# Kernel tuning notes

Measured on AMD Instinct MI355X. Metric: run time of the kernel, lower is better.

The kernel has to match this reference:

```python
import jax, jax.numpy as jnp
import numpy as np

B, L, DM, DH = 8, 2048, 1024, 1024


def setup_inputs() -> dict:
    key = jax.random.key(0)
    ks = jax.random.split(key, 10)
    s_dm = 1.0 / np.sqrt(DM)   # nn.Linear(d_model, *) init bound
    s_dh = 1.0 / np.sqrt(DH)   # nn.Linear(d_hidden, *) init bound
    u = lambda k, shp, s: jax.random.uniform(k, shp, jnp.float32, -s, s)
    return {
        "x": jax.random.normal(ks[0], (B, L, DM), jnp.float32),
        # A scaled by 0.01 so cumprod(exp(delta*A)) stays finite over L=2048
        "A": 0.01 * jax.random.normal(ks[1], (DH,), jnp.float32),
        "Bw": u(ks[2], (DH, DM), s_dm), "Bb": u(ks[3], (DH,), s_dm),
        "Cw": u(ks[4], (DM, DH), s_dh), "Cb": u(ks[5], (DM,), s_dh),
        "Dw": u(ks[6], (DM, DM), s_dm), "Db": u(ks[7], (DM,), s_dm),
        "dw": u(ks[8], (DH, DM), s_dm), "db": u(ks[9], (DH,), s_dm),
    }


def reference(x, A, Bw, Bb, Cw, Cb, Dw, Db, dw, db):
    # x: [B, L, DM]
    delta = jax.nn.softplus(jnp.einsum('bld,hd->blh', x, dw) + db)   # [B,L,DH]
    A_bar = jnp.exp(delta * A)                                        # [B,L,DH]
    B_bar = delta * (jnp.einsum('bld,hd->blh', x, Bw) + Bb)           # [B,L,DH]
    A_cum = jnp.cumprod(A_bar, axis=1)                                # [B,L,DH]
    h = jnp.cumsum(B_bar / A_cum, axis=1) * A_cum                     # [B,L,DH]
    out = jnp.einsum('blh,dh->bld', h, Cw) + Cb \
        + jnp.einsum('bld,ed->ble', x, Dw) + Db                       # [B,L,DM]
    return out
```

## Files before the change

### kernel.cpp

```cpp
#include <hip/hip_runtime.h>
#include <hip/hip_bf16.h>
#include <stdint.h>

#define DMODEL 1024
#define DHID   1024
#define NBATCH 8
#define LSEQ   2048
#define MROWS  (NBATCH * LSEQ)
#define KCAT   2048
#define CH     32
#define NCH    64
#define BH     (NBATCH * DHID)
#define CPT    4

typedef __attribute__((ext_vector_type(8))) short  short8;
typedef __attribute__((ext_vector_type(4))) short  s16x4;
typedef __attribute__((ext_vector_type(8))) __bf16 bf16x8;
typedef __attribute__((ext_vector_type(4))) float  f32x4;

__device__ __forceinline__ unsigned short f2bf(float f) {
  union { float f; unsigned int u; } v; v.f = f;
  unsigned int u = v.u;
  u += 0x7fffu + ((u >> 16) & 1u);
  return (unsigned short)(u >> 16);
}

__device__ __forceinline__ float bf2f(unsigned short s) {
  union { unsigned int u; float f; } v; v.u = ((unsigned int)s) << 16;
  return v.f;
}

__device__ __forceinline__ float softplus_f(float x) {
  return fmaxf(x, 0.f) + log1pf(expf(-fabsf(x)));
}

__device__ __forceinline__ short8 pack8(float4 a, float4 b) {
  short8 o;
  o[0] = (short)f2bf(a.x); o[1] = (short)f2bf(a.y);
  o[2] = (short)f2bf(a.z); o[3] = (short)f2bf(a.w);
  o[4] = (short)f2bf(b.x); o[5] = (short)f2bf(b.y);
  o[6] = (short)f2bf(b.z); o[7] = (short)f2bf(b.w);
  return o;
}

__global__ __launch_bounds__(256)
void cast_all_kernel(const float* __restrict__ x,
                     const float* __restrict__ dw, const float* __restrict__ Bw,
                     const float* __restrict__ Cw, const float* __restrict__ Dw,
                     unsigned short* __restrict__ A2,
                     unsigned short* __restrict__ W1, unsigned short* __restrict__ W2) {
  const size_t MX = (size_t)MROWS * 1024;
  const size_t M1 = (size_t)1024 * 1024;
  size_t i8 = ((size_t)blockIdx.x * 256 + threadIdx.x) * 8;
  if (i8 < MX) {
    size_t row = i8 >> 10; int col = (int)(i8 & 1023);
    const float4* p = (const float4*)(x + i8);
    *(short8*)(A2 + row * (size_t)KCAT + 1024 + col) = pack8(p[0], p[1]);
  } else if (i8 < MX + 2 * M1) {
    size_t k = i8 - MX;
    const float* src = (k < M1) ? (dw + k) : (Bw + k - M1);
    const float4* p = (const float4*)src;
    *(short8*)(W1 + k) = pack8(p[0], p[1]);
  } else {
    size_t k = i8 - MX - 2 * M1;
    size_t d = k >> 11; int c = (int)(k & 2047);
    const float* src = (c < 1024) ? (Cw + d * 1024 + c) : (Dw + d * 1024 + (c - 1024));
    const float4* p = (const float4*)src;
    *(short8*)(W2 + k) = pack8(p[0], p[1]);
  }
}

__device__ __forceinline__ void stage_tile(const unsigned short* g0, int ld,
                                           unsigned short* s0, int t, int lane) {
#pragma unroll
  for (int half = 0; half < 2; ++half) {
    int c = t + half * 256;
    const unsigned short* g = g0 + (size_t)(c >> 2) * ld + (c & 3) * 8;
    unsigned short* s = s0 + ((size_t)(t - lane) + half * 256) * 8;
    __builtin_amdgcn_global_load_lds(
        (const __attribute__((address_space(1))) unsigned int*)g,
        (__attribute__((address_space(3))) unsigned int*)s, 16, 0, 0);
  }
}

__global__ __launch_bounds__(256, 4)
void gemm_bt(const unsigned short* __restrict__ A, int lda,
             const unsigned short* __restrict__ B, int ldb,
             void* __restrict__ Cp, int ldc, int K, int mode,
             const float* __restrict__ bias0, const float* __restrict__ bias1) {
  __shared__ __align__(16) unsigned short As[128 * 32];
  __shared__ __align__(16) unsigned short Bs[128 * 32];
  const int t = threadIdx.x;
  const int lane = t & 63, wave = t >> 6;
  const int quad = lane >> 4, l16 = lane & 15;

  const int Nt = gridDim.x, Mt = gridDim.y;
  int bid = blockIdx.y * Nt + blockIdx.x;
  int xcd = bid & 7;
  int slot = bid >> 3;
  int lm = slot / Nt;
  int ln = slot - lm * Nt;
  const int m0 = (xcd * (Mt >> 3) + lm) * 128;
  const int n0 = ln * 128;

  const int wm = (wave & 1) * 64, wn = (wave >> 1) * 64;

  const unsigned short* Ab = A + (size_t)m0 * lda;
  const unsigned short* Bb = B + (size_t)n0 * ldb;

  f32x4 acc[4][4] = {};

  for (int k0 = 0; k0 < K; k0 += 32) {
    stage_tile(Ab + k0, lda, As, t, lane);
    stage_tile(Bb + k0, ldb, Bs, t, lane);
    __syncthreads();
    short8 af[4], bfr[4];
#pragma unroll
    for (int i = 0; i < 4; ++i)
      af[i] = *(const short8*)(As + ((size_t)(wm + i * 16 + l16)) * 32 + quad * 8);
#pragma unroll
    for (int j = 0; j < 4; ++j)
      bfr[j] = *(const short8*)(Bs + ((size_t)(wn + j * 16 + l16)) * 32 + quad * 8);
#pragma unroll
    for (int i = 0; i < 4; ++i)
#pragma unroll
      for (int j = 0; j < 4; ++j)
        acc[i][j] = __builtin_amdgcn_mfma_f32_16x16x32_bf16(
            __builtin_bit_cast(bf16x8, af[i]),
            __builtin_bit_cast(bf16x8, bfr[j]), acc[i][j], 0, 0, 0);
    __syncthreads();
  }

  if (mode == 0) {
    float* C = (float*)Cp;
#pragma unroll
    for (int i = 0; i < 4; ++i)
#pragma unroll
      for (int j = 0; j < 4; ++j) {
        int n = n0 + wn + j * 16 + l16;
        int mb = m0 + wm + i * 16 + quad * 4;
        float badd = bias0[n] + bias1[n];
#pragma unroll
        for (int r = 0; r < 4; ++r)
          C[(size_t)(mb + r) * ldc + n] = acc[i][j][r] + badd;
      }
  } else {
    unsigned short* C16 = (unsigned short*)Cp;
#pragma unroll
    for (int i = 0; i < 4; ++i)
#pragma unroll
      for (int j = 0; j < 4; ++j) {
        int n = n0 + wn + j * 16 + l16;
        int mb = m0 + wm + i * 16 + quad * 4;
#pragma unroll
        for (int r = 0; r < 4; ++r)
          C16[(size_t)(mb + r) * ldc + n] = f2bf(acc[i][j][r]);
      }
  }
}

__global__ __launch_bounds__(256)
void scan_carry_kernel(unsigned short* __restrict__ G1,
                       const float* __restrict__ Av, const float* __restrict__ Bbv,
                       const float* __restrict__ dbv, float2* __restrict__ carr) {
  int t = blockIdx.x * 256 + threadIdx.x;
  int ho = t & 255, chunk = (t >> 8) & (NCH - 1), b = t >> 14;
  int h0 = ho << 2;
  float4 A0 = *(const float4*)(Av + h0);
  float4 B0 = *(const float4*)(Bbv + h0);
  float4 D0 = *(const float4*)(dbv + h0);
  float Ah[4]  = {A0.x, A0.y, A0.z, A0.w};
  float Bbh[4] = {B0.x, B0.y, B0.z, B0.w};
  float dbh[4] = {D0.x, D0.y, D0.z, D0.w};
  unsigned short* base = G1 + ((size_t)(b * LSEQ + chunk * CH)) * KCAT + h0;
  float hs[4] = {}, sd[4] = {};
  s16x4 dp = *(const s16x4*)(base);
  s16x4 bp = *(const s16x4*)(base + 1024);
#pragma unroll 4
  for (int l = 0; l < CH; ++l) {
    s16x4 dpn = dp, bpn = bp;
    if (l + 1 < CH) {
      dpn = *(const s16x4*)(base + (size_t)(l + 1) * KCAT);
      bpn = *(const s16x4*)(base + (size_t)(l + 1) * KCAT + 1024);
    }
    s16x4 dq, bq;
#pragma unroll
    for (int j = 0; j < 4; ++j) {
      float d = softplus_f(bf2f((unsigned short)dp[j]) + dbh[j]);
      unsigned short dr = f2bf(d);
      float drf = bf2f(dr);
      float bb = drf * (bf2f((unsigned short)bp[j]) + Bbh[j]);
      unsigned short br = f2bf(bb);
      sd[j] += drf;
      float a = __expf(drf * Ah[j]);
      hs[j] = fmaf(a, hs[j], bf2f(br));
      dq[j] = (short)dr; bq[j] = (short)br;
    }
    *(s16x4*)(base + (size_t)l * KCAT) = dq;
    *(s16x4*)(base + (size_t)l * KCAT + 1024) = bq;
    dp = dpn; bp = bpn;
  }
  float2* cb = carr + (size_t)chunk * BH + b * 1024 + h0;
#pragma unroll
  for (int j = 0; j < 4; ++j)
    cb[j] = make_float2(__expf(Ah[j] * sd[j]), hs[j]);
}

__global__ __launch_bounds__(256)
void scan_comb_kernel(const float2* __restrict__ carr, float* __restrict__ Hc) {
  int t = blockIdx.x * 256 + threadIdx.x;
  float H = 0.f;
#pragma unroll
  for (int c = 0; c < NCH; ++c) {
    float2 ah = carr[(size_t)c * BH + t];
    Hc[(size_t)c * BH + t] = H;
    H = fmaf(ah.x, H, ah.y);
  }
}

__global__ __launch_bounds__(256)
void scan_final_kernel(const unsigned short* __restrict__ G1,
                       const float* __restrict__ Av, const float* __restrict__ Hc,
                       unsigned short* __restrict__ A2) {
  int t = blockIdx.x * 256 + threadIdx.x;
  int ho = t & 255, chunk = (t >> 8) & (NCH - 1), b = t >> 14;
  int h0 = ho << 2;
  float4 A0 = *(const float4*)(Av + h0);
  float Ah[4] = {A0.x, A0.y, A0.z, A0.w};
  const unsigned short* base = G1 + ((size_t)(b * LSEQ + chunk * CH)) * KCAT + h0;
  unsigned short* obase = A2 + ((size_t)(b * LSEQ + chunk * CH)) * KCAT + h0;
  const float* hb = Hc + (size_t)chunk * BH + b * 1024 + h0;
  float hs[4];
#pragma unroll
  for (int j = 0; j < 4; ++j) hs[j] = hb[j];
  s16x4 dp = *(const s16x4*)(base);
  s16x4 bp = *(const s16x4*)(base + 1024);
#pragma unroll 4
  for (int l = 0; l < CH; ++l) {
    s16x4 dpn = dp, bpn = bp;
    if (l + 1 < CH) {
      dpn = *(const s16x4*)(base + (size_t)(l + 1) * KCAT);
      bpn = *(const s16x4*)(base + (size_t)(l + 1) * KCAT + 1024);
    }
    s16x4 o;
#pragma unroll
    for (int j = 0; j < 4; ++j) {
      float d = bf2f((unsigned short)dp[j]);
      float a = __expf(d * Ah[j]);
      hs[j] = fmaf(a, hs[j], bf2f((unsigned short)bp[j]));
      o[j] = (short)f2bf(hs[j]);
    }
    *(s16x4*)(obase + (size_t)l * KCAT) = o;
    dp = dpn; bp = bpn;
  }
}

extern "C" void kernel_launch(void* const* d_in, const int* in_sizes, int n_in,
                              void* d_out, int out_size, void* d_ws, size_t ws_size,
                              hipStream_t stream) {
  const float* x  = (const float*)d_in[0];
  const float* Av = (const float*)d_in[1];
  const float* Bw = (const float*)d_in[2];
  const float* Bb = (const float*)d_in[3];
  const float* Cw = (const float*)d_in[4];
  const float* Cb = (const float*)d_in[5];
  const float* Dw = (const float*)d_in[6];
  const float* Db = (const float*)d_in[7];
  const float* dw = (const float*)d_in[8];
  const float* db = (const float*)d_in[9];
  float* out = (float*)d_out;

  const size_t sz_big = (size_t)MROWS * KCAT * 2;
  const size_t sz_w   = (size_t)2048 * 1024 * 2;
  const size_t sz_hc  = (size_t)NCH * BH * 4;
  const size_t need = 2 * sz_big + 2 * sz_w + sz_hc;
  if (ws_size < need) return;

  char* w = (char*)d_ws;
  unsigned short* A2 = (unsigned short*)w; w += sz_big;
  unsigned short* G1 = (unsigned short*)w; w += sz_big;
  unsigned short* W1 = (unsigned short*)w; w += sz_w;
  unsigned short* W2 = (unsigned short*)w; w += sz_w;
  float* Hc = (float*)w;                   w += sz_hc;
  float2* carr = (float2*)W1;

  const size_t cast_elems = (size_t)MROWS * 1024 + 2 * (size_t)2048 * 1024;
  cast_all_kernel<<<(int)(cast_elems / (256 * 8)), 256, 0, stream>>>(
      x, dw, Bw, Cw, Dw, A2, W1, W2);

  dim3 g1(KCAT / 128, MROWS / 128);
  gemm_bt<<<g1, 256, 0, stream>>>(A2 + 1024, KCAT, W1, 1024, G1, KCAT, 1024, 1,
                                  nullptr, nullptr);

  scan_carry_kernel<<<(NBATCH * NCH * (DHID / CPT)) / 256, 256, 0, stream>>>(
      G1, Av, Bb, db, carr);
  scan_comb_kernel<<<BH / 256, 256, 0, stream>>>(carr, Hc);
  scan_final_kernel<<<(NBATCH * NCH * (DHID / CPT)) / 256, 256, 0, stream>>>(
      G1, Av, Hc, A2);

  dim3 g2(DMODEL / 128, MROWS / 128);
  gemm_bt<<<g2, 256, 0, stream>>>(A2, KCAT, W2, KCAT, out, DMODEL, KCAT, 0, Cb, Db);
}
```

Measured before the change: 392.7 us.

## Replace GEMM with 256x256-tile, 8-wave, 4-stage LDS-pipelined kernel

Replaces the 128x128 single-buffered GEMM with a 256x256 tile kernel using 512 threads. It runs a 4-buffer LDS ring with three k-tiles prefetched through global_load_lds, and paces it with explicit vmcnt waits, raw s_barrier and setprio around the MFMA blocks. Operands are staged in a fragment-major layout so each lane reads its 16-byte fragment contiguously. The aim is to hide global load latency and raise data reuse per tile. In exchange it uses 128KB of LDS per block and a larger accumulator register footprint, with fewer blocks in flight.

```diff
diff --git a/kernel.cpp b/kernel.cpp
--- a/kernel.cpp
+++ b/kernel.cpp
@@ -70,91 +70,125 @@
   }
 }
 
-__device__ __forceinline__ void stage_tile(const unsigned short* g0, int ld,
-                                           unsigned short* s0, int t, int lane) {
-#pragma unroll
-  for (int half = 0; half < 2; ++half) {
-    int c = t + half * 256;
-    const unsigned short* g = g0 + (size_t)(c >> 2) * ld + (c & 3) * 8;
-    unsigned short* s = s0 + ((size_t)(t - lane) + half * 256) * 8;
+
+__device__ __forceinline__ void stage_frag32(const unsigned short* __restrict__ gbase,
+                                             int ld, int k0,
+                                             unsigned short* sbase,
+                                             int wave, int quad, int l16) {
+#pragma unroll
+  for (int s = 0; s < 2; ++s) {
+    int f = s * 8 + wave;
+    const unsigned short* g = gbase + (size_t)(f * 16 + l16) * ld + k0 + quad * 8;
+    unsigned short* sd = sbase + (size_t)(s * 512 + wave * 64) * 8;
     __builtin_amdgcn_global_load_lds(
         (const __attribute__((address_space(1))) unsigned int*)g,
-        (__attribute__((address_space(3))) unsigned int*)s, 16, 0, 0);
-  }
-}
-
-__global__ __launch_bounds__(256, 4)
-void gemm_bt(const unsigned short* __restrict__ A, int lda,
+        (__attribute__((address_space(3))) unsigned int*)sd, 16, 0, 0);
+  }
+}
+
+__global__ __launch_bounds__(512, 2)
+void gemm256(const unsigned short* __restrict__ A, int lda,
              const unsigned short* __restrict__ B, int ldb,
              void* __restrict__ Cp, int ldc, int K, int mode,
              const float* __restrict__ bias0, const float* __restrict__ bias1) {
-  __shared__ __align__(16) unsigned short As[128 * 32];
-  __shared__ __align__(16) unsigned short Bs[128 * 32];
-  const int t = threadIdx.x;
-  const int lane = t & 63, wave = t >> 6;
+  __shared__ __align__(16) unsigned short smem[4 * 16384];
+  const int tid  = threadIdx.x;
+  const int lane = tid & 63;
+  const int wave = tid >> 6;
+  const int wr   = wave >> 2;
+  const int wc   = wave & 3;
   const int quad = lane >> 4, l16 = lane & 15;
 
   const int Nt = gridDim.x, Mt = gridDim.y;
-  int bid = blockIdx.y * Nt + blockIdx.x;
-  int xcd = bid & 7;
+  int bid  = blockIdx.y * Nt + blockIdx.x;
+  int xcd  = bid & 7;
   int slot = bid >> 3;
   int lm = slot / Nt;
   int ln = slot - lm * Nt;
-  const int m0 = (xcd * (Mt >> 3) + lm) * 128;
-  const int n0 = ln * 128;
-
-  const int wm = (wave & 1) * 64, wn = (wave >> 1) * 64;
+  const int m0 = (xcd * (Mt >> 3) + lm) * 256;
+  const int n0 = ln * 256;
 
   const unsigned short* Ab = A + (size_t)m0 * lda;
   const unsigned short* Bb = B + (size_t)n0 * ldb;
 
-  f32x4 acc[4][4] = {};
-
-  for (int k0 = 0; k0 < K; k0 += 32) {
-    stage_tile(Ab + k0, lda, As, t, lane);
-    stage_tile(Bb + k0, ldb, Bs, t, lane);
-    __syncthreads();
-    short8 af[4], bfr[4];
-#pragma unroll
-    for (int i = 0; i < 4; ++i)
-      af[i] = *(const short8*)(As + ((size_t)(wm + i * 16 + l16)) * 32 + quad * 8);
-#pragma unroll
-    for (int j = 0; j < 4; ++j)
-      bfr[j] = *(const short8*)(Bs + ((size_t)(wn + j * 16 + l16)) * 32 + quad * 8);
-#pragma unroll
-    for (int i = 0; i < 4; ++i)
+  const int nt = K >> 5;
+
+  f32x4 acc[8][4] = {};
+
+#pragma unroll
+  for (int t = 0; t < 3; ++t) {
+    unsigned short* buf = smem + t * 16384;
+    stage_frag32(Ab, lda, t * 32, buf, wave, quad, l16);
+    stage_frag32(Bb, ldb, t * 32, buf + 8192, wave, quad, l16);
+  }
+  asm volatile("s_waitcnt vmcnt(8)" ::: "memory");
+  __builtin_amdgcn_s_barrier();
+  __builtin_amdgcn_sched_barrier(0);
+
+  for (int t = 0; t < nt; ++t) {
+    const unsigned short* As = smem + (t & 3) * 16384;
+    const unsigned short* Bs = As + 8192;
+    unsigned short* nbuf = smem + ((t + 3) & 3) * 16384;
+    const bool pf = (t + 3) < nt;
+    const int kpf = (t + 3) * 32;
+#pragma unroll
+    for (int ph = 0; ph < 2; ++ph) {
+      short8 af[4], bfr[4];
+#pragma unroll
+      for (int i = 0; i < 4; ++i)
+        af[i] = *(const short8*)(As + (size_t)(wr * 8 + ph * 4 + i) * 512 + lane * 8);
 #pragma unroll
       for (int j = 0; j < 4; ++j)
-        acc[i][j] = __builtin_amdgcn_mfma_f32_16x16x32_bf16(
-            __builtin_bit_cast(bf16x8, af[i]),
-            __builtin_bit_cast(bf16x8, bfr[j]), acc[i][j], 0, 0, 0);
-    __syncthreads();
+        bfr[j] = *(const short8*)(Bs + (size_t)(wc * 4 + j) * 512 + lane * 8);
+      if (pf) {
+        if (ph == 0) stage_frag32(Ab, lda, kpf, nbuf, wave, quad, l16);
+        else         stage_frag32(Bb, ldb, kpf, nbuf + 8192, wave, quad, l16);
+      }
+      __builtin_amdgcn_s_barrier();
+      __builtin_amdgcn_sched_barrier(0);
+      __builtin_amdgcn_s_setprio(1);
+#pragma unroll
+      for (int i = 0; i < 4; ++i)
+#pragma unroll
+        for (int j = 0; j < 4; ++j)
+          acc[ph * 4 + i][j] = __builtin_amdgcn_mfma_f32_16x16x32_bf16(
+              __builtin_bit_cast(bf16x8, af[i]),
+              __builtin_bit_cast(bf16x8, bfr[j]), acc[ph * 4 + i][j], 0, 0, 0);
+      __builtin_amdgcn_s_setprio(0);
+      if (ph == 1) {
+        if (t + 3 < nt)      { asm volatile("s_waitcnt vmcnt(8)" ::: "memory"); }
+        else if (t + 2 < nt) { asm volatile("s_waitcnt vmcnt(4)" ::: "memory"); }
+        else if (t + 1 < nt) { asm volatile("s_waitcnt vmcnt(0)" ::: "memory"); }
+      }
+      __builtin_amdgcn_s_barrier();
+      __builtin_amdgcn_sched_barrier(0);
+    }
   }
 
   if (mode == 0) {
     float* C = (float*)Cp;
 #pragma unroll
-    for (int i = 0; i < 4; ++i)
+    for (int mi = 0; mi < 8; ++mi)
 #pragma unroll
       for (int j = 0; j < 4; ++j) {
-        int n = n0 + wn + j * 16 + l16;
-        int mb = m0 + wm + i * 16 + quad * 4;
+        int n  = n0 + wc * 64 + j * 16 + l16;
+        int mb = m0 + wr * 128 + mi * 16 + quad * 4;
         float badd = bias0[n] + bias1[n];
 #pragma unroll
         for (int r = 0; r < 4; ++r)
-          C[(size_t)(mb + r) * ldc + n] = acc[i][j][r] + badd;
+          C[(size_t)(mb + r) * ldc + n] = acc[mi][j][r] + badd;
       }
   } else {
     unsigned short* C16 = (unsigned short*)Cp;
 #pragma unroll
-    for (int i = 0; i < 4; ++i)
+    for (int mi = 0; mi < 8; ++mi)
 #pragma unroll
       for (int j = 0; j < 4; ++j) {
-        int n = n0 + wn + j * 16 + l16;
-        int mb = m0 + wm + i * 16 + quad * 4;
+        int n  = n0 + wc * 64 + j * 16 + l16;
+        int mb = m0 + wr * 128 + mi * 16 + quad * 4;
 #pragma unroll
         for (int r = 0; r < 4; ++r)
-          C16[(size_t)(mb + r) * ldc + n] = f2bf(acc[i][j][r]);
+          C16[(size_t)(mb + r) * ldc + n] = f2bf(acc[mi][j][r]);
       }
   }
 }
@@ -288,8 +322,8 @@
   cast_all_kernel<<<(int)(cast_elems / (256 * 8)), 256, 0, stream>>>(
       x, dw, Bw, Cw, Dw, A2, W1, W2);
 
-  dim3 g1(KCAT / 128, MROWS / 128);
-  gemm_bt<<<g1, 256, 0, stream>>>(A2 + 1024, KCAT, W1, 1024, G1, KCAT, 1024, 1,
+  dim3 g1(KCAT / 256, MROWS / 256);
+  gemm256<<<g1, 512, 0, stream>>>(A2 + 1024, KCAT, W1, 1024, G1, KCAT, 1024, 1,
                                   nullptr, nullptr);
 
   scan_carry_kernel<<<(NBATCH * NCH * (DHID / CPT)) / 256, 256, 0, stream>>>(
@@ -298,6 +332,6 @@
   scan_final_kernel<<<(NBATCH * NCH * (DHID / CPT)) / 256, 256, 0, stream>>>(
       G1, Av, Hc, A2);
 
-  dim3 g2(DMODEL / 128, MROWS / 128);
-  gemm_bt<<<g2, 256, 0, stream>>>(A2, KCAT, W2, KCAT, out, DMODEL, KCAT, 0, Cb, Db);
-}
+  dim3 g2(DMODEL / 256, MROWS / 256);
+  gemm256<<<g2, 512, 0, stream>>>(A2, KCAT, W2, KCAT, out, DMODEL, KCAT, 0, Cb, Db);
+}
```

Result: faster. 372.1 us (-5.3%).

## Triple-buffer GEMM LDS tiles with async prefetch and fragment-ordered layout

Applied to the files above, without the earlier changes.

The bf16 MFMA GEMM now keeps three LDS stages and prefetches tiles two k-steps ahead with global_load_lds, waiting on vmcnt instead of the two __syncthreads per iteration. LDS tiles are stored in a fragment-major layout so each lane reads its short8 contiguously, which should avoid bank conflicts. The aim is to hide global-load latency behind MFMA work. In exchange, LDS use grows and occupancy is lowered to 3 blocks per CU.

```diff
diff --git a/kernel.cpp b/kernel.cpp
--- a/kernel.cpp
+++ b/kernel.cpp
@@ -70,57 +70,75 @@
   }
 }
 
-__device__ __forceinline__ void stage_tile(const unsigned short* g0, int ld,
-                                           unsigned short* s0, int t, int lane) {
-#pragma unroll
-  for (int half = 0; half < 2; ++half) {
-    int c = t + half * 256;
-    const unsigned short* g = g0 + (size_t)(c >> 2) * ld + (c & 3) * 8;
-    unsigned short* s = s0 + ((size_t)(t - lane) + half * 256) * 8;
+
+__device__ __forceinline__ void stage128(const unsigned short* __restrict__ gbase,
+                                         int ld, int k0,
+                                         unsigned short* sbase,
+                                         int wave, int quad, int l16) {
+#pragma unroll
+  for (int s = 0; s < 2; ++s) {
+    int f = s * 4 + wave;
+    const unsigned short* g = gbase + (size_t)(f * 16 + l16) * ld + k0 + quad * 8;
+    unsigned short* sd = sbase + (size_t)f * 512;
     __builtin_amdgcn_global_load_lds(
         (const __attribute__((address_space(1))) unsigned int*)g,
-        (__attribute__((address_space(3))) unsigned int*)s, 16, 0, 0);
-  }
-}
-
-__global__ __launch_bounds__(256, 4)
+        (__attribute__((address_space(3))) unsigned int*)sd, 16, 0, 0);
+  }
+}
+
+__global__ __launch_bounds__(256, 3)
 void gemm_bt(const unsigned short* __restrict__ A, int lda,
              const unsigned short* __restrict__ B, int ldb,
              void* __restrict__ Cp, int ldc, int K, int mode,
              const float* __restrict__ bias0, const float* __restrict__ bias1) {
-  __shared__ __align__(16) unsigned short As[128 * 32];
-  __shared__ __align__(16) unsigned short Bs[128 * 32];
-  const int t = threadIdx.x;
-  const int lane = t & 63, wave = t >> 6;
+  __shared__ __align__(16) unsigned short smem[3 * 8192];
+  const int tid  = threadIdx.x;
+  const int lane = tid & 63;
+  const int wave = tid >> 6;
   const int quad = lane >> 4, l16 = lane & 15;
+  const int wm = (wave & 1) * 64, wn = (wave >> 1) * 64;
 
   const int Nt = gridDim.x, Mt = gridDim.y;
-  int bid = blockIdx.y * Nt + blockIdx.x;
-  int xcd = bid & 7;
+  int bid  = blockIdx.y * Nt + blockIdx.x;
+  int xcd  = bid & 7;
   int slot = bid >> 3;
   int lm = slot / Nt;
   int ln = slot - lm * Nt;
   const int m0 = (xcd * (Mt >> 3) + lm) * 128;
   const int n0 = ln * 128;
 
-  const int wm = (wave & 1) * 64, wn = (wave >> 1) * 64;
-
   const unsigned short* Ab = A + (size_t)m0 * lda;
   const unsigned short* Bb = B + (size_t)n0 * ldb;
 
+  const int nt = K >> 5;
+
   f32x4 acc[4][4] = {};
 
-  for (int k0 = 0; k0 < K; k0 += 32) {
-    stage_tile(Ab + k0, lda, As, t, lane);
-    stage_tile(Bb + k0, ldb, Bs, t, lane);
-    __syncthreads();
+  stage128(Ab, lda, 0, smem, wave, quad, l16);
+  stage128(Bb, ldb, 0, smem + 4096, wave, quad, l16);
+  stage128(Ab, lda, 32, smem + 8192, wave, quad, l16);
+  stage128(Bb, ldb, 32, smem + 8192 + 4096, wave, quad, l16);
+  asm volatile("s_waitcnt vmcnt(4)" ::: "memory");
+  __builtin_amdgcn_s_barrier();
+  __builtin_amdgcn_sched_barrier(0);
+
+  int ci = 0;
+  int si = 2;
+  for (int t = 0; t < nt; ++t) {
+    if (t + 2 < nt) {
+      unsigned short* nb = smem + si * 8192;
+      stage128(Ab, lda, (t + 2) * 32, nb, wave, quad, l16);
+      stage128(Bb, ldb, (t + 2) * 32, nb + 4096, wave, quad, l16);
+    }
+    const unsigned short* As = smem + ci * 8192;
+    const unsigned short* Bs = As + 4096;
     short8 af[4], bfr[4];
 #pragma unroll
     for (int i = 0; i < 4; ++i)
-      af[i] = *(const short8*)(As + ((size_t)(wm + i * 16 + l16)) * 32 + quad * 8);
+      af[i] = *(const short8*)(As + (size_t)(((wave & 1) * 4 + i)) * 512 + lane * 8);
 #pragma unroll
     for (int j = 0; j < 4; ++j)
-      bfr[j] = *(const short8*)(Bs + ((size_t)(wn + j * 16 + l16)) * 32 + quad * 8);
+      bfr[j] = *(const short8*)(Bs + (size_t)(((wave >> 1) * 4 + j)) * 512 + lane * 8);
 #pragma unroll
     for (int i = 0; i < 4; ++i)
 #pragma unroll
@@ -128,7 +146,12 @@
         acc[i][j] = __builtin_amdgcn_mfma_f32_16x16x32_bf16(
             __builtin_bit_cast(bf16x8, af[i]),
             __builtin_bit_cast(bf16x8, bfr[j]), acc[i][j], 0, 0, 0);
-    __syncthreads();
+    if (t + 2 < nt)      { asm volatile("s_waitcnt vmcnt(4)" ::: "memory"); }
+    else if (t + 1 < nt) { asm volatile("s_waitcnt vmcnt(0)" ::: "memory"); }
+    __builtin_amdgcn_s_barrier();
+    __builtin_amdgcn_sched_barrier(0);
+    ci = (ci == 2) ? 0 : ci + 1;
+    si = (si == 2) ? 0 : si + 1;
   }
 
   if (mode == 0) {
@@ -137,7 +160,7 @@
     for (int i = 0; i < 4; ++i)
 #pragma unroll
       for (int j = 0; j < 4; ++j) {
-        int n = n0 + wn + j * 16 + l16;
+        int n  = n0 + wn + j * 16 + l16;
         int mb = m0 + wm + i * 16 + quad * 4;
         float badd = bias0[n] + bias1[n];
 #pragma unroll
@@ -150,7 +173,7 @@
     for (int i = 0; i < 4; ++i)
 #pragma unroll
       for (int j = 0; j < 4; ++j) {
-        int n = n0 + wn + j * 16 + l16;
+        int n  = n0 + wn + j * 16 + l16;
         int mb = m0 + wm + i * 16 + quad * 4;
 #pragma unroll
         for (int r = 0; r < 4; ++r)
```

Result: slower. 465.4 us (+18.5%).

## Fuse softplus and B_bar into GEMM1 epilogue with interleaved dw/Bw columns

Applied to the files above, without the earlier changes.

Interleaves the dw and Bw weight rows so GEMM1 outputs delta and B projections in adjacent columns. The epilogue adds both biases, applies softplus, and uses a lane shuffle to form delta*B before writing bf16. The scan carry kernel then only reads the precomputed values and no longer rewrites G1, which removes a read-modify-write pass over the large intermediate. Both scan kernels switch to a single 8-wide load per step. The epilogue now does more work per element, and the gemm mode flag value 2 must be handled in the hidden part of gemm_bt.

```diff
diff --git a/kernel.cpp b/kernel.cpp
--- a/kernel.cpp
+++ b/kernel.cpp
@@ -58,7 +58,9 @@
     *(short8*)(A2 + row * (size_t)KCAT + 1024 + col) = pack8(p[0], p[1]);
   } else if (i8 < MX + 2 * M1) {
     size_t k = i8 - MX;
-    const float* src = (k < M1) ? (dw + k) : (Bw + k - M1);
+    size_t h = k >> 11;
+    int c = (int)(k & 1023);
+    const float* src = ((k >> 10) & 1) ? (Bw + h * 1024 + c) : (dw + h * 1024 + c);
     const float4* p = (const float4*)src;
     *(short8*)(W1 + k) = pack8(p[0], p[1]);
   } else {
@@ -152,53 +154,45 @@
       for (int j = 0; j < 4; ++j) {
         int n = n0 + wn + j * 16 + l16;
         int mb = m0 + wm + i * 16 + quad * 4;
-#pragma unroll
-        for (int r = 0; r < 4; ++r)
-          C16[(size_t)(mb + r) * ldc + n] = f2bf(acc[i][j][r]);
+        int h = n >> 1;
+        bool isd = (n & 1) == 0;
+        float bias = isd ? bias0[h] : bias1[h];
+#pragma unroll
+        for (int r = 0; r < 4; ++r) {
+          float v = acc[i][j][r] + bias;
+          float d = softplus_f(v);
+          float dn = __shfl_xor(d, 1);
+          float ov = isd ? d : dn * v;
+          C16[(size_t)(mb + r) * ldc + n] = f2bf(ov);
+        }
       }
   }
 }
 
 __global__ __launch_bounds__(256)
-void scan_carry_kernel(unsigned short* __restrict__ G1,
-                       const float* __restrict__ Av, const float* __restrict__ Bbv,
-                       const float* __restrict__ dbv, float2* __restrict__ carr) {
+void scan_carry_kernel(const unsigned short* __restrict__ G1,
+                       const float* __restrict__ Av, float2* __restrict__ carr) {
   int t = blockIdx.x * 256 + threadIdx.x;
   int ho = t & 255, chunk = (t >> 8) & (NCH - 1), b = t >> 14;
   int h0 = ho << 2;
   float4 A0 = *(const float4*)(Av + h0);
-  float4 B0 = *(const float4*)(Bbv + h0);
-  float4 D0 = *(const float4*)(dbv + h0);
-  float Ah[4]  = {A0.x, A0.y, A0.z, A0.w};
-  float Bbh[4] = {B0.x, B0.y, B0.z, B0.w};
-  float dbh[4] = {D0.x, D0.y, D0.z, D0.w};
-  unsigned short* base = G1 + ((size_t)(b * LSEQ + chunk * CH)) * KCAT + h0;
+  float Ah[4] = {A0.x, A0.y, A0.z, A0.w};
+  const unsigned short* base = G1 + ((size_t)(b * LSEQ + chunk * CH)) * KCAT + 2 * h0;
   float hs[4] = {}, sd[4] = {};
-  s16x4 dp = *(const s16x4*)(base);
-  s16x4 bp = *(const s16x4*)(base + 1024);
+  short8 v = *(const short8*)(base);
 #pragma unroll 4
   for (int l = 0; l < CH; ++l) {
-    s16x4 dpn = dp, bpn = bp;
-    if (l + 1 < CH) {
-      dpn = *(const s16x4*)(base + (size_t)(l + 1) * KCAT);
-      bpn = *(const s16x4*)(base + (size_t)(l + 1) * KCAT + 1024);
+    short8 vn = v;
+    if (l + 1 < CH)
+      vn = *(const short8*)(base + (size_t)(l + 1) * KCAT);
+#pragma unroll
+    for (int j = 0; j < 4; ++j) {
+      float d  = bf2f((unsigned short)v[2 * j]);
+      float bb = bf2f((unsigned short)v[2 * j + 1]);
+      sd[j] += d;
+      hs[j] = fmaf(__expf(d * Ah[j]), hs[j], bb);
     }
-    s16x4 dq, bq;
-#pragma unroll
-    for (int j = 0; j < 4; ++j) {
-      float d = softplus_f(bf2f((unsigned short)dp[j]) + dbh[j]);
-      unsigned short dr = f2bf(d);
-      float drf = bf2f(dr);
-      float bb = drf * (bf2f((unsigned short)bp[j]) + Bbh[j]);
-      unsigned short br = f2bf(bb);
-      sd[j] += drf;
-      float a = __expf(drf * Ah[j]);
-      hs[j] = fmaf(a, hs[j], bf2f(br));
-      dq[j] = (short)dr; bq[j] = (short)br;
-    }
-    *(s16x4*)(base + (size_t)l * KCAT) = dq;
-    *(s16x4*)(base + (size_t)l * KCAT + 1024) = bq;
-    dp = dpn; bp = bpn;
+    v = vn;
   }
   float2* cb = carr + (size_t)chunk * BH + b * 1024 + h0;
 #pragma unroll
@@ -227,31 +221,28 @@
   int h0 = ho << 2;
   float4 A0 = *(const float4*)(Av + h0);
   float Ah[4] = {A0.x, A0.y, A0.z, A0.w};
-  const unsigned short* base = G1 + ((size_t)(b * LSEQ + chunk * CH)) * KCAT + h0;
+  const unsigned short* base = G1 + ((size_t)(b * LSEQ + chunk * CH)) * KCAT + 2 * h0;
   unsigned short* obase = A2 + ((size_t)(b * LSEQ + chunk * CH)) * KCAT + h0;
   const float* hb = Hc + (size_t)chunk * BH + b * 1024 + h0;
   float hs[4];
 #pragma unroll
   for (int j = 0; j < 4; ++j) hs[j] = hb[j];
-  s16x4 dp = *(const s16x4*)(base);
-  s16x4 bp = *(const s16x4*)(base + 1024);
+  short8 v = *(const short8*)(base);
 #pragma unroll 4
   for (int l = 0; l < CH; ++l) {
-    s16x4 dpn = dp, bpn = bp;
-    if (l + 1 < CH) {
-      dpn = *(const s16x4*)(base + (size_t)(l + 1) * KCAT);
-      bpn = *(const s16x4*)(base + (size_t)(l + 1) * KCAT + 1024);
-    }
+    short8 vn = v;
+    if (l + 1 < CH)
+      vn = *(const short8*)(base + (size_t)(l + 1) * KCAT);
     s16x4 o;
 #pragma unroll
     for (int j = 0; j < 4; ++j) {
-      float d = bf2f((unsigned short)dp[j]);
-      float a = __expf(d * Ah[j]);
-      hs[j] = fmaf(a, hs[j], bf2f((unsigned short)bp[j]));
+      float d  = bf2f((unsigned short)v[2 * j]);
+      float bb = bf2f((unsigned short)v[2 * j + 1]);
+      hs[j] = fmaf(__expf(d * Ah[j]), hs[j], bb);
       o[j] = (short)f2bf(hs[j]);
     }
     *(s16x4*)(obase + (size_t)l * KCAT) = o;
-    dp = dpn; bp = bpn;
+    v = vn;
   }
 }
 
@@ -289,11 +280,11 @@
       x, dw, Bw, Cw, Dw, A2, W1, W2);
 
   dim3 g1(KCAT / 128, MROWS / 128);
-  gemm_bt<<<g1, 256, 0, stream>>>(A2 + 1024, KCAT, W1, 1024, G1, KCAT, 1024, 1,
-                                  nullptr, nullptr);
+  gemm_bt<<<g1, 256, 0, stream>>>(A2 + 1024, KCAT, W1, 1024, G1, KCAT, 1024, 2,
+                                  db, Bb);
 
   scan_carry_kernel<<<(NBATCH * NCH * (DHID / CPT)) / 256, 256, 0, stream>>>(
-      G1, Av, Bb, db, carr);
+      G1, Av, carr);
   scan_comb_kernel<<<BH / 256, 256, 0, stream>>>(carr, Hc);
   scan_final_kernel<<<(NBATCH * NCH * (DHID / CPT)) / 256, 256, 0, stream>>>(
       G1, Av, Hc, A2);
```

New measurement: 395.5 us. About the same (+0.7%).
